# Optimization experiments

Hardware: AMD Instinct MI355X
Metric: run time of the kernel (lower is better)

The kernel has to match this reference:

```python
import jax, jax.numpy as jnp
import numpy as np

VOCAB = 256
PAD = 0
D_MODEL = 512
ATTN_DIM = 64
B, L = 8, 2048
LN_EPS = 1e-5


def layer_norm(x, g, b):
    mu = jnp.mean(x, axis=-1, keepdims=True)
    var = jnp.mean(jnp.square(x - mu), axis=-1, keepdims=True)
    return (x - mu) * jax.lax.rsqrt(var + LN_EPS) * g + b


def setup_inputs() -> dict:
    key = jax.random.key(0)
    ks = jax.random.split(key, 10)
    tokens = jax.random.randint(ks[0], (B, L), 1, VOCAB)  # avoid PAD=0
    prefix_lens = jax.random.randint(ks[1], (B,), 256, 1536)
    embed_w = jax.random.normal(ks[2], (VOCAB, D_MODEL), jnp.float32) * 0.02
    embed_w = embed_w.at[PAD].set(0.0)  # padding_idx row
    en_g = jnp.ones((D_MODEL,), jnp.float32)
    en_b = jnp.zeros((D_MODEL,), jnp.float32)
    fn_g = jnp.ones((D_MODEL,), jnp.float32)
    fn_b = jnp.zeros((D_MODEL,), jnp.float32)
    q_w = jax.random.normal(ks[3], (ATTN_DIM, D_MODEL), jnp.float32) * 0.02
    q_b = jnp.zeros((ATTN_DIM,), jnp.float32)
    k_w = jax.random.normal(ks[4], (ATTN_DIM, D_MODEL), jnp.float32) * 0.02
    k_b = jnp.zeros((ATTN_DIM,), jnp.float32)
    g_w = jax.random.normal(ks[5], (1, D_MODEL), jnp.float32) * 0.02
    g_b = jnp.full((1,), 2.0, jnp.float32)  # gate bias init to 2.0
    return dict(tokens=tokens, prefix_lens=prefix_lens, embed_w=embed_w,
                en_g=en_g, en_b=en_b, fn_g=fn_g, fn_b=fn_b,
                q_w=q_w, q_b=q_b, k_w=k_w, k_b=k_b, g_w=g_w, g_b=g_b)


def reference(tokens, prefix_lens, embed_w, en_g, en_b, fn_g, fn_b,
              q_w, q_b, k_w, k_b, g_w, g_b):
    # encode (n_layers=0: embed -> embed_norm -> final_norm)
    x = embed_w[tokens]                       # (B, L, D)
    x = layer_norm(x, en_g, en_b)
    h = layer_norm(x, fn_g, fn_b)

    vocab_logits = jnp.einsum('bld,vd->blv', h, embed_w)   # tied head
    q = h @ q_w.T + q_b                       # (B, L, A)
    k = h @ k_w.T + k_b                       # (B, L, A)
    scores = jnp.einsum('btd,bsd->bts', q, k) / np.sqrt(ATTN_DIM).astype(np.float32)

    idx = jnp.arange(L)[None, :]              # (1, L)
    prefix_mask = (idx < prefix_lens[:, None]) & (tokens != PAD)  # (B, L)
    scores = jnp.where(prefix_mask[:, None, :], scores, -jnp.inf)
    attn = jax.nn.softmax(scores, axis=-1)    # (B, L, L)

    prefix_onehot = jax.nn.one_hot(tokens, VOCAB, dtype=jnp.float32)
    prefix_onehot = prefix_onehot * prefix_mask[..., None]
    copy_dist = jnp.einsum('bts,bsv->btv', attn, prefix_onehot)  # (B, L, V)

    gate = jax.nn.sigmoid(h @ g_w.T + g_b)    # (B, L, 1)
    vocab_probs = jax.nn.softmax(vocab_logits, axis=-1)
    mixed = gate * vocab_probs + (1.0 - gate) * copy_dist
    mixed = jnp.clip(mixed, 1e-12, None)
    return jnp.log(mixed), gate[..., 0], attn
```

## Files before the change

### kernel.cpp

```cpp
#include <hip/hip_runtime.h>
#include <math.h>


#define DM 512
#define VC 256
#define SL 2048
#define NB 8
#define AD 64

__device__ __forceinline__ float wave_sum(float v) {
#pragma unroll
  for (int o = 32; o > 0; o >>= 1) v += __shfl_xor(v, o, 64);
  return v;
}
__device__ __forceinline__ float wave_max(float v) {
#pragma unroll
  for (int o = 32; o > 0; o >>= 1) v = fmaxf(v, __shfl_xor(v, o, 64));
  return v;
}
__device__ __forceinline__ float blk_sum(float v, float* red) {
  v = wave_sum(v);
  if ((threadIdx.x & 63) == 0) red[threadIdx.x >> 6] = v;
  __syncthreads();
  float r = red[0] + red[1] + red[2] + red[3];
  __syncthreads();
  return r;
}
__device__ __forceinline__ float blk_max(float v, float* red) {
  v = wave_max(v);
  if ((threadIdx.x & 63) == 0) red[threadIdx.x >> 6] = v;
  __syncthreads();
  float r = fmaxf(fmaxf(red[0], red[1]), fmaxf(red[2], red[3]));
  __syncthreads();
  return r;
}

__global__ __launch_bounds__(256) void ktok_pre(
    const float* __restrict__ embed_w,
    const float* __restrict__ en_g, const float* __restrict__ en_b,
    const float* __restrict__ fn_g, const float* __restrict__ fn_b,
    const float* __restrict__ q_w, const float* __restrict__ q_b,
    const float* __restrict__ k_w, const float* __restrict__ k_b,
    const float* __restrict__ g_w, const float* __restrict__ g_b,
    float* __restrict__ h_tok, float* __restrict__ q_tok,
    float* __restrict__ k_tok, float* __restrict__ gate_tok,
    float* __restrict__ probs_tok)
{
  __shared__ float red[4];
  __shared__ float hs[DM];
  const int tt = blockIdx.x;
  const int tid = threadIdx.x;

  float x0 = embed_w[tt * DM + tid];
  float x1 = embed_w[tt * DM + 256 + tid];
  float mu = blk_sum(x0 + x1, red) * (1.0f / DM);
  float d0 = x0 - mu, d1 = x1 - mu;
  float var = blk_sum(d0 * d0 + d1 * d1, red) * (1.0f / DM);
  float inv = 1.0f / sqrtf(var + 1e-5f);
  float y0 = d0 * inv * en_g[tid] + en_b[tid];
  float y1 = d1 * inv * en_g[tid + 256] + en_b[tid + 256];
  mu = blk_sum(y0 + y1, red) * (1.0f / DM);
  d0 = y0 - mu; d1 = y1 - mu;
  var = blk_sum(d0 * d0 + d1 * d1, red) * (1.0f / DM);
  inv = 1.0f / sqrtf(var + 1e-5f);
  float h0 = d0 * inv * fn_g[tid] + fn_b[tid];
  float h1 = d1 * inv * fn_g[tid + 256] + fn_b[tid + 256];
  hs[tid] = h0; hs[tid + 256] = h1;
  h_tok[tt * DM + tid] = h0;
  h_tok[tt * DM + 256 + tid] = h1;
  float gp = blk_sum(h0 * g_w[tid] + h1 * g_w[tid + 256], red);
  if (tid == 0) gate_tok[tt] = 1.0f / (1.0f + expf(-(gp + g_b[0])));
  if (tid < 128) {
    int a = tid & 63;
    const float* w = (tid < 64 ? q_w : k_w) + a * DM;
    float acc = 0.0f;
    for (int d = 0; d < DM; ++d) acc += hs[d] * w[d];
    if (tid < 64) q_tok[tt * AD + a] = acc + q_b[a];
    else          k_tok[tt * AD + a] = acc + k_b[a];
  }
  const float* ev = embed_w + tid * DM;
  float logit = 0.0f;
  for (int d = 0; d < DM; ++d) logit += hs[d] * ev[d];
  float m = blk_max(logit, red);
  float e = expf(logit - m);
  float Z = blk_sum(e, red);
  probs_tok[tt * VC + tid] = e / Z;
}

__global__ __launch_bounds__(256) void kscores(
    const float* __restrict__ q_tok, const float* __restrict__ k_tok,
    float* __restrict__ S)
{
  __shared__ float qr[AD];
  int tt = blockIdx.x, tid = threadIdx.x;
  if (tid < AD) qr[tid] = q_tok[tt * AD + tid];
  __syncthreads();
  const float* kr = k_tok + tid * AD;
  float acc = 0.0f;
#pragma unroll
  for (int a = 0; a < AD; ++a) acc += qr[a] * kr[a];
  S[tt * VC + tid] = acc * 0.125f;
}

__global__ __launch_bounds__(256) void khist(
    const int* __restrict__ tokens, const int* __restrict__ prefix_lens,
    int* __restrict__ cnt)
{
  __shared__ int c[VC];
  int b = blockIdx.x, tid = threadIdx.x;
  c[tid] = 0;
  __syncthreads();
  int P = prefix_lens[b];
  for (int s = tid; s < SL; s += 256) {
    if (s < P) {
      int t = tokens[b * SL + s];
      if (t != 0) atomicAdd(&c[t], 1);
    }
  }
  __syncthreads();
  cnt[b * VC + tid] = c[tid];
}

__global__ __launch_bounds__(256) void ktables(
    const float* __restrict__ S, const int* __restrict__ cnt,
    const float* __restrict__ gate_tok, const float* __restrict__ probs_tok,
    float* __restrict__ e_norm, float* __restrict__ logmix)
{
  __shared__ float red[4];
  int b = blockIdx.x >> 8, tt = blockIdx.x & 255;
  int v = threadIdx.x;
  float sv = S[tt * VC + v];
  int c = cnt[b * VC + v];
  float m = blk_max(c > 0 ? sv : -1e30f, red);
  float e = expf(sv - m);
  float Z = blk_sum((float)c * e, red);
  float en = e / Z;
  int idx = (b * VC + tt) * VC + v;
  e_norm[idx] = en;
  float g = gate_tok[tt];
  float mixed = g * probs_tok[tt * VC + v] + (1.0f - g) * ((float)c * en);
  logmix[idx] = logf(fmaxf(mixed, 1e-12f));
}

__global__ __launch_bounds__(256) void kwrite(
    const int* __restrict__ tokens, const int* __restrict__ prefix_lens,
    const float* __restrict__ e_norm, const float* __restrict__ logmix,
    const float* __restrict__ gate_tok,
    float* __restrict__ out_logmix, float* __restrict__ out_gate,
    float* __restrict__ out_attn)
{
  __shared__ float erow[VC];
  int row = blockIdx.x;
  int b = row >> 11;
  int tid = threadIdx.x;
  int tt = tokens[row];
  int base = (b * VC + tt) * VC;
  erow[tid] = e_norm[base + tid];
  out_logmix[(size_t)row * VC + tid] = logmix[base + tid];
  if (tid == 0) out_gate[row] = gate_tok[tt];
  int P = prefix_lens[b];
  __syncthreads();
  const int4* tokrow = (const int4*)(tokens + b * SL);
  float4* arow = (float4*)(out_attn + (size_t)row * SL);
  for (int i = tid; i < SL / 4; i += 256) {
    int4 tk = tokrow[i];
    int s0 = i * 4;
    float4 val;
    val.x = (s0     < P && tk.x != 0) ? erow[tk.x] : 0.0f;
    val.y = (s0 + 1 < P && tk.y != 0) ? erow[tk.y] : 0.0f;
    val.z = (s0 + 2 < P && tk.z != 0) ? erow[tk.z] : 0.0f;
    val.w = (s0 + 3 < P && tk.w != 0) ? erow[tk.w] : 0.0f;
    arow[i] = val;
  }
}

extern "C" void kernel_launch(void* const* d_in, const int* in_sizes, int n_in,
                              void* d_out, int out_size, void* d_ws, size_t ws_size,
                              hipStream_t stream)
{
  const int*   tokens      = (const int*)  d_in[0];
  const int*   prefix_lens = (const int*)  d_in[1];
  const float* embed_w     = (const float*)d_in[2];
  const float* en_g        = (const float*)d_in[3];
  const float* en_b        = (const float*)d_in[4];
  const float* fn_g        = (const float*)d_in[5];
  const float* fn_b        = (const float*)d_in[6];
  const float* q_w         = (const float*)d_in[7];
  const float* q_b         = (const float*)d_in[8];
  const float* k_w         = (const float*)d_in[9];
  const float* k_b         = (const float*)d_in[10];
  const float* g_w         = (const float*)d_in[11];
  const float* g_b         = (const float*)d_in[12];

  float* ws        = (float*)d_ws;
  float* h_tok     = ws;
  float* q_tok     = h_tok + 256 * 512;
  float* k_tok     = q_tok + 256 * 64;
  float* gate_tok  = k_tok + 256 * 64;
  float* probs_tok = gate_tok + 256;
  float* S         = probs_tok + 256 * 256;
  int*   cnt       = (int*)(S + 256 * 256);
  float* e_norm    = (float*)(cnt + 8 * 256);
  float* logmix    = e_norm + 8 * 256 * 256;

  float* out_logmix = (float*)d_out;
  float* out_gate   = out_logmix + (size_t)NB * SL * VC;
  float* out_attn   = out_gate + (size_t)NB * SL;

  ktok_pre<<<256, 256, 0, stream>>>(embed_w, en_g, en_b, fn_g, fn_b,
      q_w, q_b, k_w, k_b, g_w, g_b, h_tok, q_tok, k_tok, gate_tok, probs_tok);
  kscores<<<256, 256, 0, stream>>>(q_tok, k_tok, S);
  khist<<<NB, 256, 0, stream>>>(tokens, prefix_lens, cnt);
  ktables<<<NB * 256, 256, 0, stream>>>(S, cnt, gate_tok, probs_tok, e_norm, logmix);
  kwrite<<<NB * SL, 256, 0, stream>>>(tokens, prefix_lens, e_norm, logmix,
      gate_tok, out_logmix, out_gate, out_attn);
}
```

Measured before the change: 229.4 us.

## Pre-transpose weights for coalesced dot products, fuse scores into tables, stream attn stores

```diff
diff --git a/kernel.cpp b/kernel.cpp
--- a/kernel.cpp
+++ b/kernel.cpp
@@ -8,6 +8,8 @@
 #define NB 8
 #define AD 64
 
+typedef float f4v __attribute__((ext_vector_type(4)));
+
 __device__ __forceinline__ float wave_sum(float v) {
 #pragma unroll
   for (int o = 32; o > 0; o >>= 1) v += __shfl_xor(v, o, 64);
@@ -35,19 +37,51 @@
   return r;
 }
 
-__global__ __launch_bounds__(256) void ktok_pre(
+__global__ __launch_bounds__(256) void kprep(
+    const float* __restrict__ embed_w, const float* __restrict__ q_w,
+    const float* __restrict__ k_w, const int* __restrict__ tokens,
+    const int* __restrict__ prefix_lens,
+    float* __restrict__ embed_P, float* __restrict__ qk_P,
+    int* __restrict__ cnt)
+{
+  __shared__ int c[VC];
+  const int blk = blockIdx.x;
+  const int tid = threadIdx.x;
+  if (blk < DM) {
+    const int d = blk;
+    embed_P[(((d >> 2) * VC + tid) << 2) + (d & 3)] = embed_w[tid * DM + d];
+    if (tid < 128) {
+      float val = (tid < 64) ? q_w[tid * DM + d] : k_w[(tid - 64) * DM + d];
+      qk_P[(((d >> 2) * 128 + tid) << 2) + (d & 3)] = val;
+    }
+  } else {
+    const int b = blk - DM;
+    c[tid] = 0;
+    __syncthreads();
+    const int P = prefix_lens[b];
+    for (int s = tid; s < SL; s += 256) {
+      if (s < P) {
+        int t = tokens[b * SL + s];
+        if (t != 0) atomicAdd(&c[t], 1);
+      }
+    }
+    __syncthreads();
+    cnt[b * VC + tid] = c[tid];
+  }
+}
+
+__global__ __launch_bounds__(256) void ktok(
     const float* __restrict__ embed_w,
     const float* __restrict__ en_g, const float* __restrict__ en_b,
     const float* __restrict__ fn_g, const float* __restrict__ fn_b,
-    const float* __restrict__ q_w, const float* __restrict__ q_b,
-    const float* __restrict__ k_w, const float* __restrict__ k_b,
+    const float* __restrict__ q_b, const float* __restrict__ k_b,
     const float* __restrict__ g_w, const float* __restrict__ g_b,
-    float* __restrict__ h_tok, float* __restrict__ q_tok,
-    float* __restrict__ k_tok, float* __restrict__ gate_tok,
-    float* __restrict__ probs_tok)
+    const float* __restrict__ embed_P, const float* __restrict__ qk_P,
+    float* __restrict__ q_tok, float* __restrict__ kT_P,
+    float* __restrict__ gate_tok, float* __restrict__ probs_tok)
 {
   __shared__ float red[4];
-  __shared__ float hs[DM];
+  __shared__ __align__(16) float hs[DM];
   const int tt = blockIdx.x;
   const int tid = threadIdx.x;
 
@@ -66,70 +100,62 @@
   float h0 = d0 * inv * fn_g[tid] + fn_b[tid];
   float h1 = d1 * inv * fn_g[tid + 256] + fn_b[tid + 256];
   hs[tid] = h0; hs[tid + 256] = h1;
-  h_tok[tt * DM + tid] = h0;
-  h_tok[tt * DM + 256 + tid] = h1;
   float gp = blk_sum(h0 * g_w[tid] + h1 * g_w[tid + 256], red);
   if (tid == 0) gate_tok[tt] = 1.0f / (1.0f + expf(-(gp + g_b[0])));
+
+  const float4* hs4 = (const float4*)hs;
   if (tid < 128) {
-    int a = tid & 63;
-    const float* w = (tid < 64 ? q_w : k_w) + a * DM;
+    const float4* w4p = (const float4*)qk_P;
     float acc = 0.0f;
-    for (int d = 0; d < DM; ++d) acc += hs[d] * w[d];
-    if (tid < 64) q_tok[tt * AD + a] = acc + q_b[a];
-    else          k_tok[tt * AD + a] = acc + k_b[a];
-  }
-  const float* ev = embed_w + tid * DM;
-  float logit = 0.0f;
-  for (int d = 0; d < DM; ++d) logit += hs[d] * ev[d];
-  float m = blk_max(logit, red);
-  float e = expf(logit - m);
+#pragma unroll 8
+    for (int d4 = 0; d4 < DM / 4; ++d4) {
+      float4 h4 = hs4[d4];
+      float4 w4 = w4p[d4 * 128 + tid];
+      acc += h4.x * w4.x + h4.y * w4.y + h4.z * w4.z + h4.w * w4.w;
+    }
+    if (tid < 64) {
+      q_tok[tt * AD + tid] = acc + q_b[tid];
+    } else {
+      int a = tid - 64;
+      kT_P[(((a >> 2) * VC + tt) << 2) + (a & 3)] = acc + k_b[a];
+    }
+  }
+  const float4* e4p = (const float4*)embed_P;
+  float lt = 0.0f;
+#pragma unroll 8
+  for (int d4 = 0; d4 < DM / 4; ++d4) {
+    float4 h4 = hs4[d4];
+    float4 e4 = e4p[d4 * VC + tid];
+    lt += h4.x * e4.x + h4.y * e4.y + h4.z * e4.z + h4.w * e4.w;
+  }
+  float m = blk_max(lt, red);
+  float e = expf(lt - m);
   float Z = blk_sum(e, red);
   probs_tok[tt * VC + tid] = e / Z;
 }
 
-__global__ __launch_bounds__(256) void kscores(
-    const float* __restrict__ q_tok, const float* __restrict__ k_tok,
-    float* __restrict__ S)
-{
-  __shared__ float qr[AD];
-  int tt = blockIdx.x, tid = threadIdx.x;
-  if (tid < AD) qr[tid] = q_tok[tt * AD + tid];
-  __syncthreads();
-  const float* kr = k_tok + tid * AD;
-  float acc = 0.0f;
-#pragma unroll
-  for (int a = 0; a < AD; ++a) acc += qr[a] * kr[a];
-  S[tt * VC + tid] = acc * 0.125f;
-}
-
-__global__ __launch_bounds__(256) void khist(
-    const int* __restrict__ tokens, const int* __restrict__ prefix_lens,
-    int* __restrict__ cnt)
-{
-  __shared__ int c[VC];
-  int b = blockIdx.x, tid = threadIdx.x;
-  c[tid] = 0;
-  __syncthreads();
-  int P = prefix_lens[b];
-  for (int s = tid; s < SL; s += 256) {
-    if (s < P) {
-      int t = tokens[b * SL + s];
-      if (t != 0) atomicAdd(&c[t], 1);
-    }
-  }
-  __syncthreads();
-  cnt[b * VC + tid] = c[tid];
-}
-
 __global__ __launch_bounds__(256) void ktables(
-    const float* __restrict__ S, const int* __restrict__ cnt,
-    const float* __restrict__ gate_tok, const float* __restrict__ probs_tok,
+    const float* __restrict__ q_tok, const float* __restrict__ kT_P,
+    const int* __restrict__ cnt, const float* __restrict__ gate_tok,
+    const float* __restrict__ probs_tok,
     float* __restrict__ e_norm, float* __restrict__ logmix)
 {
   __shared__ float red[4];
-  int b = blockIdx.x >> 8, tt = blockIdx.x & 255;
-  int v = threadIdx.x;
-  float sv = S[tt * VC + v];
+  __shared__ __align__(16) float qs[AD];
+  const int b = blockIdx.x >> 8, tt = blockIdx.x & 255;
+  const int v = threadIdx.x;
+  if (v < AD) qs[v] = q_tok[tt * AD + v];
+  __syncthreads();
+  const float4* qs4 = (const float4*)qs;
+  const float4* k4p = (const float4*)kT_P;
+  float sv = 0.0f;
+#pragma unroll
+  for (int a4 = 0; a4 < AD / 4; ++a4) {
+    float4 q4 = qs4[a4];
+    float4 k4 = k4p[a4 * VC + v];
+    sv += q4.x * k4.x + q4.y * k4.y + q4.z * k4.z + q4.w * k4.w;
+  }
+  sv *= 0.125f;
   int c = cnt[b * VC + v];
   float m = blk_max(c > 0 ? sv : -1e30f, red);
   float e = expf(sv - m);
@@ -150,27 +176,29 @@
     float* __restrict__ out_attn)
 {
   __shared__ float erow[VC];
-  int row = blockIdx.x;
-  int b = row >> 11;
-  int tid = threadIdx.x;
-  int tt = tokens[row];
-  int base = (b * VC + tt) * VC;
+  const int row = blockIdx.x;
+  const int b = row >> 11;
+  const int tid = threadIdx.x;
+  const int tt = tokens[row];
+  const int base = (b * VC + tt) * VC;
   erow[tid] = e_norm[base + tid];
   out_logmix[(size_t)row * VC + tid] = logmix[base + tid];
   if (tid == 0) out_gate[row] = gate_tok[tt];
-  int P = prefix_lens[b];
+  const int P = prefix_lens[b];
   __syncthreads();
   const int4* tokrow = (const int4*)(tokens + b * SL);
-  float4* arow = (float4*)(out_attn + (size_t)row * SL);
-  for (int i = tid; i < SL / 4; i += 256) {
+  f4v* arow = (f4v*)(out_attn + (size_t)row * SL);
+#pragma unroll
+  for (int it = 0; it < 2; ++it) {
+    int i = tid + it * 256;
     int4 tk = tokrow[i];
     int s0 = i * 4;
-    float4 val;
+    f4v val;
     val.x = (s0     < P && tk.x != 0) ? erow[tk.x] : 0.0f;
     val.y = (s0 + 1 < P && tk.y != 0) ? erow[tk.y] : 0.0f;
     val.z = (s0 + 2 < P && tk.z != 0) ? erow[tk.z] : 0.0f;
     val.w = (s0 + 3 < P && tk.w != 0) ? erow[tk.w] : 0.0f;
-    arow[i] = val;
+    __builtin_nontemporal_store(val, &arow[i]);
   }
 }
 
@@ -185,33 +213,35 @@
   const float* en_b        = (const float*)d_in[4];
   const float* fn_g        = (const float*)d_in[5];
   const float* fn_b        = (const float*)d_in[6];
+  const float* q_b         = (const float*)d_in[8];
+  const float* k_b         = (const float*)d_in[10];
   const float* q_w         = (const float*)d_in[7];
-  const float* q_b         = (const float*)d_in[8];
   const float* k_w         = (const float*)d_in[9];
-  const float* k_b         = (const float*)d_in[10];
   const float* g_w         = (const float*)d_in[11];
   const float* g_b         = (const float*)d_in[12];
 
   float* ws        = (float*)d_ws;
-  float* h_tok     = ws;
-  float* q_tok     = h_tok + 256 * 512;
-  float* k_tok     = q_tok + 256 * 64;
-  float* gate_tok  = k_tok + 256 * 64;
-  float* probs_tok = gate_tok + 256;
-  float* S         = probs_tok + 256 * 256;
-  int*   cnt       = (int*)(S + 256 * 256);
-  float* e_norm    = (float*)(cnt + 8 * 256);
-  float* logmix    = e_norm + 8 * 256 * 256;
+  float* embed_P   = ws;
+  float* qk_P      = embed_P + DM * VC;
+  float* kT_P      = qk_P + DM * 128;
+  float* q_tok     = kT_P + AD * VC;
+  float* gate_tok  = q_tok + VC * AD;
+  float* probs_tok = gate_tok + VC;
+  int*   cnt       = (int*)(probs_tok + VC * VC);
+  float* e_norm    = (float*)(cnt + NB * VC);
+  float* logmix    = e_norm + NB * VC * VC;
 
   float* out_logmix = (float*)d_out;
   float* out_gate   = out_logmix + (size_t)NB * SL * VC;
   float* out_attn   = out_gate + (size_t)NB * SL;
 
-  ktok_pre<<<256, 256, 0, stream>>>(embed_w, en_g, en_b, fn_g, fn_b,
-      q_w, q_b, k_w, k_b, g_w, g_b, h_tok, q_tok, k_tok, gate_tok, probs_tok);
-  kscores<<<256, 256, 0, stream>>>(q_tok, k_tok, S);
-  khist<<<NB, 256, 0, stream>>>(tokens, prefix_lens, cnt);
-  ktables<<<NB * 256, 256, 0, stream>>>(S, cnt, gate_tok, probs_tok, e_norm, logmix);
+  kprep<<<DM + NB, 256, 0, stream>>>(embed_w, q_w, k_w, tokens, prefix_lens,
+                                     embed_P, qk_P, cnt);
+  ktok<<<VC, 256, 0, stream>>>(embed_w, en_g, en_b, fn_g, fn_b, q_b, k_b,
+                               g_w, g_b, embed_P, qk_P,
+                               q_tok, kT_P, gate_tok, probs_tok);
+  ktables<<<NB * VC, 256, 0, stream>>>(q_tok, kT_P, cnt, gate_tok, probs_tok,
+                                       e_norm, logmix);
   kwrite<<<NB * SL, 256, 0, stream>>>(tokens, prefix_lens, e_norm, logmix,
-      gate_tok, out_logmix, out_gate, out_attn);
-}
+                                      gate_tok, out_logmix, out_gate, out_attn);
+}
```

Result: faster. 217.9 us (-5.0%).
